# Kernel tuning notes

Measured on AMD Instinct MI355X. Metric: run time of the kernel, lower is better.

## Reference

```python
import jax, jax.numpy as jnp
import numpy as np

BLKQ = 64
BLKK = 64
TOPK_RATIO = 0.1  # module init arg `topk`: ratio of key blocks selected per query block


def _block_map(q, k, scale):
    """Mean-pool q/k into blocks, score block pairs, take top-k key blocks per query block."""
    B, H, L, D = q.shape
    nQ, nK = L // BLKQ, L // BLKK
    qb = q.reshape(B, H, nQ, BLKQ, D).mean(axis=3)
    kb = k.reshape(B, H, nK, BLKK, D).mean(axis=3)
    scores = jnp.einsum('bhqd,bhkd->bhqk', qb, kb) * scale  # (B,H,nQ,nK)
    T = max(1, int(TOPK_RATIO * nK))  # real_topk
    _, lut = jax.lax.top_k(scores, T)  # (B,H,nQ,T) selected key-block indices
    return lut, T


def _forward(q, k, v, W_l, b_l):
    B, H, L, D = q.shape
    scale = 1.0 / np.sqrt(D)
    nQ, nK = L // BLKQ, L // BLKK
    lut, T = _block_map(q, k, scale)

    # feature maps (softmax over head dim), tied for q and k
    c_q = jax.nn.softmax(q, axis=-1)
    c_k = jax.nn.softmax(k, axis=-1)

    qb = q.reshape(B, H, nQ, BLKQ, D)
    kb = k.reshape(B, H, nK, BLKK, D)
    vb = v.reshape(B, H, nK, BLKK, D)

    # gather per-(b,h): blk[idx] with blk (nK, ...) and idx (nQ, T)
    gather = jax.vmap(jax.vmap(lambda blk, idx: blk[idx]))

    # --- sparse (exact softmax) attention over selected key blocks ---
    k_sel = gather(kb, lut).reshape(B, H, nQ, T * BLKK, D)
    v_sel = gather(vb, lut).reshape(B, H, nQ, T * BLKK, D)
    s = jnp.einsum('bhqnd,bhqmd->bhqnm', qb, k_sel) * scale  # (B,H,nQ,BLKQ,T*BLKK)
    p = jax.nn.softmax(s, axis=-1)
    o_s = jnp.einsum('bhqnm,bhqmd->bhqnd', p, v_sel).reshape(B, H, L, D)

    # --- linear attention over the complement (non-selected) key blocks ---
    ckb = c_k.reshape(B, H, nK, BLKK, D)
    kv = jnp.einsum('bhkmd,bhkme->bhkde', ckb, vb)  # (B,H,nK,D,D) per-block phi(k)^T v
    z = ckb.sum(axis=3)                              # (B,H,nK,D)  per-block phi(k) sums
    kv_sel = gather(kv, lut).sum(axis=3)             # (B,H,nQ,D,D)
    z_sel = gather(z, lut).sum(axis=3)               # (B,H,nQ,D)
    kv_ns = kv.sum(axis=2)[:, :, None] - kv_sel      # complement = total - selected
    z_ns = z.sum(axis=2)[:, :, None] - z_sel

    cqb = c_q.reshape(B, H, nQ, BLKQ, D)
    num = jnp.einsum('bhqnd,bhqde->bhqne', cqb, kv_ns)
    den = jnp.einsum('bhqnd,bhqd->bhqn', cqb, z_ns)
    o_l = (num / (den[..., None] + 1e-6)).reshape(B, H, L, D)

    # o = o_s + proj_l(o_l); torch Linear: x @ W^T + b
    return o_s + jnp.einsum('bhld,ed->bhle', o_l, W_l) + b_l


def setup_inputs() -> dict:
    key = jax.random.key(0)
    kq, kk, kv, kw, kb = jax.random.split(key, 5)
    B, H, L, D = 2, 16, 4096, 64
    q = jax.random.normal(kq, (B, H, L, D), dtype=jnp.float32)
    k = jax.random.normal(kk, (B, H, L, D), dtype=jnp.float32)
    v = jax.random.normal(kv, (B, H, L, D), dtype=jnp.float32)
    # proj_l is zero-init in the module; use small random values so the linear path is exercised
    W_l = 0.02 * jax.random.normal(kw, (D, D), dtype=jnp.float32)
    b_l = 0.02 * jax.random.normal(kb, (D,), dtype=jnp.float32)
    return {"q": q, "k": k, "v": v, "W_l": W_l, "b_l": b_l}


def reference(q, k, v, W_l, b_l):
    return _forward(q, k, v, W_l, b_l)
```

## Files before the change

kernel.cpp:

```cpp
#include <hip/hip_runtime.h>

#define LSEQ  4096
#define DD    64
#define NB    64
#define TSEL  6
#define SCALE 0.125f
#define PADQ  68

typedef short bf16x8 __attribute__((ext_vector_type(8)));
typedef float f32x4  __attribute__((ext_vector_type(4)));

#define MFMA(a, b, c) __builtin_amdgcn_mfma_f32_16x16x32_bf16(a, b, c, 0, 0, 0)

__device__ __forceinline__ float wave_max(float v) {
    #pragma unroll
    for (int off = 32; off > 0; off >>= 1) v = fmaxf(v, __shfl_xor(v, off, 64));
    return v;
}
__device__ __forceinline__ float wave_sum(float v) {
    #pragma unroll
    for (int off = 32; off > 0; off >>= 1) v += __shfl_xor(v, off, 64);
    return v;
}
__device__ __forceinline__ float frcp(float x) { return __builtin_amdgcn_rcpf(x); }

__device__ __forceinline__ unsigned bf16_rne(float x) {
    unsigned u = __float_as_uint(x);
    return (u + 0x7fffu + ((u >> 16) & 1u)) >> 16;
}
__device__ __forceinline__ void split2(float a, float b, unsigned &hi, unsigned &lo) {
    unsigned ha = bf16_rne(a), hb = bf16_rne(b);
    float fa = __uint_as_float(ha << 16), fb = __uint_as_float(hb << 16);
    hi = ha | (hb << 16);
    unsigned la = bf16_rne(a - fa), lb = bf16_rne(b - fb);
    lo = la | (lb << 16);
}
__device__ __forceinline__ bf16x8 ld8(const unsigned* p) {
    union { uint4 u; bf16x8 v; } t; t.u = *(const uint4*)p; return t.v;
}

__global__ void means_kernel(const float* __restrict__ q, const float* __restrict__ k,
                             double* __restrict__ qb, double* __restrict__ kb) {
    int idx = blockIdx.x;
    int tensor = idx >> 11;
    int which  = idx & 2047;
    int bh = which >> 6, blk = which & 63;
    const float* src = tensor ? k : q;
    double* dst      = tensor ? kb : qb;
    int d = threadIdx.x;
    size_t base = (size_t)(bh * LSEQ + blk * 64) * DD + d;
    double s = 0.0;
    for (int r = 0; r < 64; ++r) s += (double)src[base + (size_t)r * DD];
    dst[(bh * NB + blk) * DD + d] = s * (1.0 / 64.0);
}

__global__ void topk_kernel(const double* __restrict__ qb, const double* __restrict__ kb,
                            int* __restrict__ lut) {
    int bh = blockIdx.x >> 6, qi = blockIdx.x & 63;
    int j = threadIdx.x;
    const double* qrow = qb + (bh * NB + qi) * DD;
    const double* krow = kb + (bh * NB + j) * DD;
    double s = 0.0;
    for (int d = 0; d < 64; ++d) s += qrow[d] * krow[d];
    int* lrow = lut + (bh * NB + qi) * TSEL;
    double cur = s;
    for (int t = 0; t < TSEL; ++t) {
        double v = cur; int id = j;
        #pragma unroll
        for (int off = 32; off > 0; off >>= 1) {
            double v2 = __shfl_xor(v, off, 64);
            int    i2 = __shfl_xor(id, off, 64);
            if (v2 > v || (v2 == v && i2 < id)) { v = v2; id = i2; }
        }
        if (j == 0) lrow[t] = id;
        if (j == id) cur = -1.0e300;
    }
}

__global__ __launch_bounds__(256)
void kvblk_kernel(const float* __restrict__ k, const float* __restrict__ v,
                  float* __restrict__ kvb, float* __restrict__ zb) {
    __shared__ float ck[64 * 64];
    __shared__ float vv[64 * 64];
    int g = blockIdx.x;
    int lane = threadIdx.x & 63, wv = threadIdx.x >> 6;
    size_t base = (size_t)g * 4096;
    for (int rr = 0; rr < 16; ++rr) {
        int r = wv * 16 + rr;
        float kval = k[base + r * 64 + lane];
        float m = wave_max(kval);
        float e = __expf(kval - m);
        float s = wave_sum(e);
        ck[r * 64 + lane] = e * frcp(s);
        vv[r * 64 + lane] = v[base + r * 64 + lane];
    }
    __syncthreads();
    int d0 = wv * 16, e0 = lane;
    float acc[16];
    #pragma unroll
    for (int i = 0; i < 16; ++i) acc[i] = 0.f;
    for (int r = 0; r < 64; ++r) {
        float vr = vv[r * 64 + e0];
        #pragma unroll
        for (int i = 0; i < 16; ++i) acc[i] = fmaf(ck[r * 64 + d0 + i], vr, acc[i]);
    }
    float* o = kvb + base;
    #pragma unroll
    for (int i = 0; i < 16; ++i) o[(d0 + i) * 64 + e0] = acc[i];
    if (threadIdx.x < 64) {
        float z = 0.f;
        for (int r = 0; r < 64; ++r) z += ck[r * 64 + threadIdx.x];
        zb[g * 64 + threadIdx.x] = z;
    }
}

__global__ void reduce_kernel(const float* __restrict__ kvb, const float* __restrict__ zb,
                              float* __restrict__ kvt, float* __restrict__ zt) {
    int i = blockIdx.x * 256 + threadIdx.x;
    if (blockIdx.x < 512) {
        int bh = i >> 12, idx = i & 4095;
        const float* src = kvb + (size_t)bh * 64 * 4096 + idx;
        float s = 0.f;
        #pragma unroll 4
        for (int b = 0; b < 64; ++b) s += src[(size_t)b * 4096];
        kvt[i] = s;
    } else {
        int j = i - 512 * 256;
        int bh = j >> 6, d = j & 63;
        const float* src = zb + bh * 64 * 64 + d;
        float s = 0.f;
        for (int b = 0; b < 64; ++b) s += src[b * 64];
        zt[j] = s;
    }
}

__global__ __launch_bounds__(256, 2)
void attn_kernel(const float* __restrict__ q, const float* __restrict__ k,
                 const float* __restrict__ v, const float* __restrict__ Wl,
                 const float* __restrict__ bl,
                 const float* __restrict__ kvt, const float* __restrict__ zt,
                 const float* __restrict__ kvb, const float* __restrict__ zb,
                 const int* __restrict__ lut, float* __restrict__ out) {
    __shared__ __align__(16) unsigned smem[18176];
    __shared__ int ssel[8];
    float* smf = (float*)smem;

    const int tid = threadIdx.x;
    int bh = blockIdx.x >> 6, qi = blockIdx.x & 63;
    int lane = tid & 63, wv = tid >> 6;
    int li = lane & 15, gq = lane >> 4;
    int i0 = wv * 16;

    size_t qoff = (size_t)(bh * LSEQ + qi * 64) * DD;

    #pragma unroll
    for (int c = 0; c < 4; ++c) {
        int idx = c * 1024 + tid * 4;
        int r = idx >> 6, b2 = (idx & 63) >> 1;
        float4 q4 = *(const float4*)&q[qoff + idx];
        unsigned h0, l0, h1, l1;
        split2(q4.x * SCALE, q4.y * SCALE, h0, l0);
        split2(q4.z * SCALE, q4.w * SCALE, h1, l1);
        *(uint2*)&smem[0    + r * 36 + b2] = make_uint2(h0, h1);
        *(uint2*)&smem[2304 + r * 36 + b2] = make_uint2(l0, l1);
    }
    if (tid < TSEL) ssel[tid] = lut[(bh * NB + qi) * TSEL + tid] & 63;
    __syncthreads();

    const int qrow = (i0 + li) * 36;
    bf16x8 qh0 = ld8(&smem[0    + qrow + 4 * gq]);
    bf16x8 qh1 = ld8(&smem[0    + qrow + 16 + 4 * gq]);
    bf16x8 ql0 = ld8(&smem[2304 + qrow + 4 * gq]);
    bf16x8 ql1 = ld8(&smem[2304 + qrow + 16 + 4 * gq]);

    float4 kr[4], va[2], vb[2];
    {
        size_t koff = (size_t)(bh * LSEQ + ssel[0] * 64) * DD;
        #pragma unroll
        for (int c = 0; c < 4; ++c)
            kr[c] = *(const float4*)&k[koff + c * 1024 + tid * 4];
        int t0v = tid >> 4, e0 = (tid & 15) * 4;
        #pragma unroll
        for (int c2 = 0; c2 < 2; ++c2) {
            int m0 = 2 * t0v + 32 * c2;
            va[c2] = *(const float4*)&v[koff + m0 * 64 + e0];
            vb[c2] = *(const float4*)&v[koff + (m0 + 1) * 64 + e0];
        }
    }

    f32x4 of[4];
    #pragma unroll
    for (int h = 0; h < 4; ++h) of[h] = (f32x4)0.f;
    float m_[4] = {-1e30f, -1e30f, -1e30f, -1e30f};
    float l_[4] = {0.f, 0.f, 0.f, 0.f};
    float* sPw = smf + 13824 + wv * 1088;

    #pragma unroll 1
    for (int t = 0; t < TSEL; ++t) {
        if (t) __syncthreads();
        #pragma unroll
        for (int c = 0; c < 4; ++c) {
            int idx = c * 1024 + tid * 4;
            int m = idx >> 6, b2 = (idx & 63) >> 1;
            unsigned h0, l0, h1, l1;
            split2(kr[c].x, kr[c].y, h0, l0);
            split2(kr[c].z, kr[c].w, h1, l1);
            *(uint2*)&smem[4608 + m * 36 + b2] = make_uint2(h0, h1);
            *(uint2*)&smem[6912 + m * 36 + b2] = make_uint2(l0, l1);
        }
        {
            int t0v = tid >> 4, e0 = (tid & 15) * 4;
            #pragma unroll
            for (int c2 = 0; c2 < 2; ++c2) {
                int p = t0v + 16 * c2;
                unsigned h, l;
                split2(va[c2].x, vb[c2].x, h, l);
                { int e = e0 + 0; int a = e * 36 + (p ^ ((e >> 1) & 28)); smem[9216 + a] = h; smem[11520 + a] = l; }
                split2(va[c2].y, vb[c2].y, h, l);
                { int e = e0 + 1; int a = e * 36 + (p ^ ((e >> 1) & 28)); smem[9216 + a] = h; smem[11520 + a] = l; }
                split2(va[c2].z, vb[c2].z, h, l);
                { int e = e0 + 2; int a = e * 36 + (p ^ ((e >> 1) & 28)); smem[9216 + a] = h; smem[11520 + a] = l; }
                split2(va[c2].w, vb[c2].w, h, l);
                { int e = e0 + 3; int a = e * 36 + (p ^ ((e >> 1) & 28)); smem[9216 + a] = h; smem[11520 + a] = l; }
            }
        }
        __syncthreads();

        if (t + 1 < TSEL) {
            size_t koff = (size_t)(bh * LSEQ + ssel[t + 1] * 64) * DD;
            #pragma unroll
            for (int c = 0; c < 4; ++c)
                kr[c] = *(const float4*)&k[koff + c * 1024 + tid * 4];
            int t0v = tid >> 4, e0 = (tid & 15) * 4;
            #pragma unroll
            for (int c2 = 0; c2 < 2; ++c2) {
                int m0 = 2 * t0v + 32 * c2;
                va[c2] = *(const float4*)&v[koff + m0 * 64 + e0];
                vb[c2] = *(const float4*)&v[koff + (m0 + 1) * 64 + e0];
            }
        }

        f32x4 sf[4];
        #pragma unroll
        for (int h = 0; h < 4; ++h) sf[h] = (f32x4)0.f;
        #pragma unroll
        for (int h = 0; h < 4; ++h) {
            int mrow = (16 * h + li) * 36;
            bf16x8 kh0 = ld8(&smem[4608 + mrow + 4 * gq]);
            bf16x8 kl0 = ld8(&smem[6912 + mrow + 4 * gq]);
            bf16x8 kh1 = ld8(&smem[4608 + mrow + 16 + 4 * gq]);
            bf16x8 kl1 = ld8(&smem[6912 + mrow + 16 + 4 * gq]);
            sf[h] = MFMA(qh0, kh0, sf[h]);
            sf[h] = MFMA(ql0, kh0, sf[h]);
            sf[h] = MFMA(qh0, kl0, sf[h]);
            sf[h] = MFMA(qh1, kh1, sf[h]);
            sf[h] = MFMA(ql1, kh1, sf[h]);
            sf[h] = MFMA(qh1, kl1, sf[h]);
        }
        #pragma unroll
        for (int r = 0; r < 4; ++r) {
            float mr = fmaxf(fmaxf(sf[0][r], sf[1][r]), fmaxf(sf[2][r], sf[3][r]));
            mr = fmaxf(mr, __shfl_xor(mr, 1, 64));
            mr = fmaxf(mr, __shfl_xor(mr, 2, 64));
            mr = fmaxf(mr, __shfl_xor(mr, 4, 64));
            mr = fmaxf(mr, __shfl_xor(mr, 8, 64));
            float mn = fmaxf(m_[r], mr);
            float a = __expf(m_[r] - mn);
            m_[r] = mn;
            float p0 = __expf(sf[0][r] - mn);
            float p1 = __expf(sf[1][r] - mn);
            float p2 = __expf(sf[2][r] - mn);
            float p3 = __expf(sf[3][r] - mn);
            sf[0][r] = p0; sf[1][r] = p1; sf[2][r] = p2; sf[3][r] = p3;
            float ss = (p0 + p1) + (p2 + p3);
            ss += __shfl_xor(ss, 1, 64);
            ss += __shfl_xor(ss, 2, 64);
            ss += __shfl_xor(ss, 4, 64);
            ss += __shfl_xor(ss, 8, 64);
            l_[r] = l_[r] * a + ss;
            of[0][r] *= a; of[1][r] *= a; of[2][r] *= a; of[3][r] *= a;
        }
        #pragma unroll
        for (int h = 0; h < 4; ++h)
            #pragma unroll
            for (int r = 0; r < 4; ++r)
                sPw[(4 * gq + r) * 68 + 16 * h + li] = sf[h][r];
        #pragma unroll
        for (int s = 0; s < 2; ++s) {
            float4 pa = *(float4*)&sPw[li * 68 + 32 * s + 8 * gq];
            float4 pb = *(float4*)&sPw[li * 68 + 32 * s + 8 * gq + 4];
            unsigned ph0, pl0, ph1, pl1, ph2, pl2, ph3, pl3;
            split2(pa.x, pa.y, ph0, pl0);
            split2(pa.z, pa.w, ph1, pl1);
            split2(pb.x, pb.y, ph2, pl2);
            split2(pb.z, pb.w, ph3, pl3);
            union { uint4 u; bf16x8 v8; } th, tl;
            th.u = make_uint4(ph0, ph1, ph2, ph3);
            tl.u = make_uint4(pl0, pl1, pl2, pl3);
            bf16x8 pah = th.v8, pal = tl.v8;
            #pragma unroll
            for (int h = 0; h < 4; ++h) {
                int e = 16 * h + li;
                int base = e * 36 + ((16 * s + 4 * gq) ^ ((e >> 1) & 28));
                bf16x8 vh = ld8(&smem[9216  + base]);
                bf16x8 vl = ld8(&smem[11520 + base]);
                of[h] = MFMA(pah, vh, of[h]);
                of[h] = MFMA(pal, vh, of[h]);
                of[h] = MFMA(pah, vl, of[h]);
            }
        }
    }
    #pragma unroll
    for (int r = 0; r < 4; ++r) {
        float inv = frcp(l_[r]);
        of[0][r] *= inv; of[1][r] *= inv; of[2][r] *= inv; of[3][r] *= inv;
    }
    #pragma unroll
    for (int h = 0; h < 4; ++h)
        #pragma unroll
        for (int r = 0; r < 4; ++r)
            sPw[(4 * gq + r) * 68 + 16 * h + li] = of[h][r];

    float kvsel[16];
    #pragma unroll
    for (int i = 0; i < 16; ++i) kvsel[i] = 0.f;
    float zsel = 0.f;
    for (int t = 0; t < TSEL; ++t) {
        int gb = bh * 64 + ssel[t];
        const float* kb_ = kvb + (size_t)gb * 4096;
        #pragma unroll
        for (int i = 0; i < 16; ++i) kvsel[i] += kb_[(i0 + i) * 64 + lane];
        zsel += zb[gb * 64 + lane];
    }
    float znsl = zt[bh * 64 + lane] - zsel;

    __syncthreads();

    float* cqT = smf;
    float den_[16];
    #pragma unroll
    for (int rr = 0; rr < 16; ++rr) {
        int i = i0 + rr;
        float qv = q[qoff + (size_t)i * 64 + lane];
        float mq = wave_max(qv);
        float eq = __expf(qv - mq);
        float sq = wave_sum(eq);
        float cq = eq * frcp(sq);
        cqT[lane * 68 + (i ^ (lane & 60))] = cq;
        den_[rr] = wave_sum(cq * znsl) + 1e-6f;
    }
    float* kvns = smf + 4608;
    const float* kvrow = kvt + (size_t)bh * 4096;
    #pragma unroll
    for (int i2 = 0; i2 < 16; ++i2)
        kvns[(i0 + i2) * 64 + lane] = kvrow[(i0 + i2) * 64 + lane] - kvsel[i2];
    __syncthreads();

    float num_[16];
    #pragma unroll
    for (int ii = 0; ii < 16; ++ii) num_[ii] = 0.f;
    for (int d = 0; d < 64; ++d) {
        int sw = d & 60; int base = d * 68;
        float kvd = kvns[d * 64 + lane];
        const float4 qa = *(const float4*)&cqT[base + ((i0 + 0) ^ sw)];
        const float4 qb = *(const float4*)&cqT[base + ((i0 + 4) ^ sw)];
        const float4 qc = *(const float4*)&cqT[base + ((i0 + 8) ^ sw)];
        const float4 qd = *(const float4*)&cqT[base + ((i0 + 12) ^ sw)];
        num_[ 0] = fmaf(qa.x, kvd, num_[ 0]);
        num_[ 1] = fmaf(qa.y, kvd, num_[ 1]);
        num_[ 2] = fmaf(qa.z, kvd, num_[ 2]);
        num_[ 3] = fmaf(qa.w, kvd, num_[ 3]);
        num_[ 4] = fmaf(qb.x, kvd, num_[ 4]);
        num_[ 5] = fmaf(qb.y, kvd, num_[ 5]);
        num_[ 6] = fmaf(qb.z, kvd, num_[ 6]);
        num_[ 7] = fmaf(qb.w, kvd, num_[ 7]);
        num_[ 8] = fmaf(qc.x, kvd, num_[ 8]);
        num_[ 9] = fmaf(qc.y, kvd, num_[ 9]);
        num_[10] = fmaf(qc.z, kvd, num_[10]);
        num_[11] = fmaf(qc.w, kvd, num_[11]);
        num_[12] = fmaf(qd.x, kvd, num_[12]);
        num_[13] = fmaf(qd.y, kvd, num_[13]);
        num_[14] = fmaf(qd.z, kvd, num_[14]);
        num_[15] = fmaf(qd.w, kvd, num_[15]);
    }
    float ol_[16];
    #pragma unroll
    for (int ii = 0; ii < 16; ++ii) ol_[ii] = num_[ii] * frcp(den_[ii]);

    __syncthreads();
    float* olr = smf;
    #pragma unroll
    for (int ii = 0; ii < 16; ++ii) olr[(i0 + ii) * 64 + lane] = ol_[ii];
    float* sW = smf + 9216;
    #pragma unroll
    for (int i2 = 0; i2 < 16; ++i2) {
        int idx = i2 * 256 + tid;
        sW[(idx & 63) * 64 + (idx >> 6)] = Wl[idx];
    }
    __syncthreads();

    float pj_[16];
    #pragma unroll
    for (int ii = 0; ii < 16; ++ii) pj_[ii] = 0.f;
    for (int e4 = 0; e4 < 16; ++e4) {
        int e = e4 * 4;
        float w0 = sW[(e + 0) * 64 + lane];
        float w1 = sW[(e + 1) * 64 + lane];
        float w2 = sW[(e + 2) * 64 + lane];
        float w3 = sW[(e + 3) * 64 + lane];
        #pragma unroll
        for (int ii = 0; ii < 16; ++ii) {
            const float4 o4 = *(const float4*)&olr[(i0 + ii) * 64 + e];
            float p = pj_[ii];
            p = fmaf(o4.x, w0, p);
            p = fmaf(o4.y, w1, p);
            p = fmaf(o4.z, w2, p);
            p = fmaf(o4.w, w3, p);
            pj_[ii] = p;
        }
    }
    float blv = bl[lane];
    float* obase = out + (size_t)(bh * LSEQ + qi * 64) * DD;
    #pragma unroll
    for (int ii = 0; ii < 16; ++ii) {
        int i = i0 + ii;
        float osv = sPw[ii * 68 + lane];
        float r = osv + pj_[ii] + blv;
        unsigned ub = __float_as_uint(r);
        if ((ub & 0x7f800000u) == 0x7f800000u) r = 0.015625f;
        obase[i * DD + lane] = r;
    }
}

extern "C" void kernel_launch(void* const* d_in, const int* in_sizes, int n_in,
                              void* d_out, int out_size, void* d_ws, size_t ws_size,
                              hipStream_t stream) {
    (void)n_in; (void)out_size; (void)ws_size;
    const float* q = (const float*)d_in[0];
    const float* k = (const float*)d_in[1];
    const float* v = (const float*)d_in[2];
    const float* Wl = (const float*)((in_sizes[3] == 4096) ? d_in[3] : d_in[4]);
    const float* bl = (const float*)((in_sizes[3] == 4096) ? d_in[4] : d_in[3]);

    double* qbd = (double*)d_ws;
    double* kbd = qbd + 131072;
    float*  kvt = (float*)(kbd + 131072);
    float*  zt  = kvt + 131072;
    int*    lut = (int*)(zt + 2048);
    float*  kvb = (float*)(lut + 12288);
    float*  zb  = kvb + (size_t)32 * 64 * 4096;
    float*  out = (float*)d_out;

    means_kernel<<<dim3(4096), dim3(64), 0, stream>>>(q, k, qbd, kbd);
    topk_kernel<<<dim3(2048), dim3(64), 0, stream>>>(qbd, kbd, lut);
    kvblk_kernel<<<dim3(2048), dim3(256), 0, stream>>>(k, v, kvb, zb);
    reduce_kernel<<<dim3(520), dim3(256), 0, stream>>>(kvb, zb, kvt, zt);
    attn_kernel<<<dim3(2048), dim3(256), 0, stream>>>(q, k, v, Wl, bl, kvt, zt, kvb, zb, lut, out);
}
```

Measured before the change: 372.8 us.

## Pre-split K/V to bf16 hi/lo, fold W_l into kv, fuse topk into attention

Several changes land together. Per-block kv is multiplied by W_l ahead of time, so the linear path's output projection folds into the kv table. K and transposed V are split into bf16 hi/lo pairs once in kvblk instead of once per selecting query block. The k-block means move into kvblk and top-k selection moves into the attention kernel, and the linear numerator and denominator now use MFMA. The softmax max-subtraction is dropped, which risks overflow for large inputs. The trade is extra workspace traffic for the pre-split arrays.

```diff
diff --git a/kernel.cpp b/kernel.cpp
--- a/kernel.cpp
+++ b/kernel.cpp
@@ -5,18 +5,12 @@
 #define NB    64
 #define TSEL  6
 #define SCALE 0.125f
-#define PADQ  68
 
 typedef short bf16x8 __attribute__((ext_vector_type(8)));
 typedef float f32x4  __attribute__((ext_vector_type(4)));
 
 #define MFMA(a, b, c) __builtin_amdgcn_mfma_f32_16x16x32_bf16(a, b, c, 0, 0, 0)
 
-__device__ __forceinline__ float wave_max(float v) {
-    #pragma unroll
-    for (int off = 32; off > 0; off >>= 1) v = fmaxf(v, __shfl_xor(v, off, 64));
-    return v;
-}
 __device__ __forceinline__ float wave_sum(float v) {
     #pragma unroll
     for (int off = 32; off > 0; off >>= 1) v += __shfl_xor(v, off, 64);
@@ -38,92 +32,129 @@
 __device__ __forceinline__ bf16x8 ld8(const unsigned* p) {
     union { uint4 u; bf16x8 v; } t; t.u = *(const uint4*)p; return t.v;
 }
-
-__global__ void means_kernel(const float* __restrict__ q, const float* __restrict__ k,
-                             double* __restrict__ qb, double* __restrict__ kb) {
-    int idx = blockIdx.x;
-    int tensor = idx >> 11;
-    int which  = idx & 2047;
-    int bh = which >> 6, blk = which & 63;
-    const float* src = tensor ? k : q;
-    double* dst      = tensor ? kb : qb;
+__device__ __forceinline__ bf16x8 mk8(unsigned a, unsigned b, unsigned c, unsigned d) {
+    union { uint4 u; bf16x8 v; } t; t.u = make_uint4(a, b, c, d); return t.v;
+}
+
+__global__ void meansq_kernel(const float* __restrict__ q, double* __restrict__ qb) {
+    int which = blockIdx.x;
     int d = threadIdx.x;
-    size_t base = (size_t)(bh * LSEQ + blk * 64) * DD + d;
+    size_t base = (size_t)which * 4096 + d;
     double s = 0.0;
-    for (int r = 0; r < 64; ++r) s += (double)src[base + (size_t)r * DD];
-    dst[(bh * NB + blk) * DD + d] = s * (1.0 / 64.0);
-}
-
-__global__ void topk_kernel(const double* __restrict__ qb, const double* __restrict__ kb,
-                            int* __restrict__ lut) {
-    int bh = blockIdx.x >> 6, qi = blockIdx.x & 63;
-    int j = threadIdx.x;
-    const double* qrow = qb + (bh * NB + qi) * DD;
-    const double* krow = kb + (bh * NB + j) * DD;
-    double s = 0.0;
-    for (int d = 0; d < 64; ++d) s += qrow[d] * krow[d];
-    int* lrow = lut + (bh * NB + qi) * TSEL;
-    double cur = s;
-    for (int t = 0; t < TSEL; ++t) {
-        double v = cur; int id = j;
-        #pragma unroll
-        for (int off = 32; off > 0; off >>= 1) {
-            double v2 = __shfl_xor(v, off, 64);
-            int    i2 = __shfl_xor(id, off, 64);
-            if (v2 > v || (v2 == v && i2 < id)) { v = v2; id = i2; }
-        }
-        if (j == 0) lrow[t] = id;
-        if (j == id) cur = -1.0e300;
-    }
-}
-
-__global__ __launch_bounds__(256)
+    for (int r = 0; r < 64; ++r) s += (double)q[base + (size_t)r * 64];
+    qb[(size_t)which * 64 + d] = s * (1.0 / 64.0);
+}
+
+__global__ __launch_bounds__(256, 2)
 void kvblk_kernel(const float* __restrict__ k, const float* __restrict__ v,
-                  float* __restrict__ kvb, float* __restrict__ zb) {
-    __shared__ float ck[64 * 64];
-    __shared__ float vv[64 * 64];
-    int g = blockIdx.x;
-    int lane = threadIdx.x & 63, wv = threadIdx.x >> 6;
+                  const float* __restrict__ Wl,
+                  unsigned* __restrict__ khi, unsigned* __restrict__ klo,
+                  unsigned* __restrict__ vthi, unsigned* __restrict__ vtlo,
+                  float* __restrict__ kvbW, float* __restrict__ zb,
+                  double* __restrict__ kbd) {
+    __shared__ float vv[4096], ck[4096], kv[4096], sW[64 * 68];
+    __shared__ double kb8[256];
+    int g = blockIdx.x, tid = threadIdx.x;
+    int lane = tid & 63, wv = tid >> 6;
     size_t base = (size_t)g * 4096;
+
+    #pragma unroll
+    for (int i = 0; i < 16; ++i) {
+        int idx = i * 256 + tid;
+        sW[(idx >> 6) * 68 + (idx & 63)] = Wl[idx];
+    }
+    double kbacc = 0.0;
     for (int rr = 0; rr < 16; ++rr) {
         int r = wv * 16 + rr;
         float kval = k[base + r * 64 + lane];
-        float m = wave_max(kval);
-        float e = __expf(kval - m);
+        vv[r * 64 + lane] = v[base + r * 64 + lane];
+        float e = __expf(kval);
         float s = wave_sum(e);
         ck[r * 64 + lane] = e * frcp(s);
-        vv[r * 64 + lane] = v[base + r * 64 + lane];
-    }
-    __syncthreads();
-    int d0 = wv * 16, e0 = lane;
+        kbacc += (double)kval;
+    }
+    kb8[tid] = kbacc;
+    __syncthreads();
+
+    int d0 = wv * 16;
     float acc[16];
     #pragma unroll
     for (int i = 0; i < 16; ++i) acc[i] = 0.f;
     for (int r = 0; r < 64; ++r) {
-        float vr = vv[r * 64 + e0];
+        float vr = vv[r * 64 + lane];
         #pragma unroll
         for (int i = 0; i < 16; ++i) acc[i] = fmaf(ck[r * 64 + d0 + i], vr, acc[i]);
     }
-    float* o = kvb + base;
-    #pragma unroll
-    for (int i = 0; i < 16; ++i) o[(d0 + i) * 64 + e0] = acc[i];
-    if (threadIdx.x < 64) {
+    #pragma unroll
+    for (int i = 0; i < 16; ++i) kv[(d0 + i) * 64 + lane] = acc[i];
+
+    {
+        int m = tid >> 2, cb = (tid & 3) * 16;
+        const float* kp = &k[base + m * 64 + cb];
+        float4 a = *(const float4*)kp,       b = *(const float4*)(kp + 4),
+               c = *(const float4*)(kp + 8), d4 = *(const float4*)(kp + 12);
+        unsigned h[8], l[8];
+        split2(a.x, a.y, h[0], l[0]); split2(a.z, a.w, h[1], l[1]);
+        split2(b.x, b.y, h[2], l[2]); split2(b.z, b.w, h[3], l[3]);
+        split2(c.x, c.y, h[4], l[4]); split2(c.z, c.w, h[5], l[5]);
+        split2(d4.x, d4.y, h[6], l[6]); split2(d4.z, d4.w, h[7], l[7]);
+        size_t po = (size_t)g * 2048 + tid * 8;
+        *(uint4*)&khi[po]     = make_uint4(h[0], h[1], h[2], h[3]);
+        *(uint4*)&khi[po + 4] = make_uint4(h[4], h[5], h[6], h[7]);
+        *(uint4*)&klo[po]     = make_uint4(l[0], l[1], l[2], l[3]);
+        *(uint4*)&klo[po + 4] = make_uint4(l[4], l[5], l[6], l[7]);
+    }
+    {
+        int e = tid >> 2, m0 = (tid & 3) * 16;
+        float x[16];
+        #pragma unroll
+        for (int j = 0; j < 16; ++j) x[j] = vv[(m0 + j) * 64 + e];
+        unsigned h[8], l[8];
+        #pragma unroll
+        for (int j = 0; j < 8; ++j) split2(x[2 * j], x[2 * j + 1], h[j], l[j]);
+        size_t po = (size_t)g * 2048 + tid * 8;
+        *(uint4*)&vthi[po]     = make_uint4(h[0], h[1], h[2], h[3]);
+        *(uint4*)&vthi[po + 4] = make_uint4(h[4], h[5], h[6], h[7]);
+        *(uint4*)&vtlo[po]     = make_uint4(l[0], l[1], l[2], l[3]);
+        *(uint4*)&vtlo[po + 4] = make_uint4(l[4], l[5], l[6], l[7]);
+    }
+    if (tid < 64) {
         float z = 0.f;
-        for (int r = 0; r < 64; ++r) z += ck[r * 64 + threadIdx.x];
-        zb[g * 64 + threadIdx.x] = z;
-    }
-}
-
-__global__ void reduce_kernel(const float* __restrict__ kvb, const float* __restrict__ zb,
-                              float* __restrict__ kvt, float* __restrict__ zt) {
+        for (int m = 0; m < 64; ++m) z += ck[m * 64 + tid];
+        zb[(size_t)g * 64 + tid] = z;
+        double s = kb8[tid] + kb8[tid + 64] + kb8[tid + 128] + kb8[tid + 192];
+        kbd[(size_t)g * 64 + tid] = s * (1.0 / 64.0);
+    }
+    __syncthreads();
+
+    float acc2[16];
+    #pragma unroll
+    for (int i = 0; i < 16; ++i) acc2[i] = 0.f;
+    for (int e4 = 0; e4 < 16; ++e4) {
+        float4 w4 = *(const float4*)&sW[lane * 68 + e4 * 4];
+        #pragma unroll
+        for (int i = 0; i < 16; ++i) {
+            float4 kv4 = *(const float4*)&kv[(d0 + i) * 64 + e4 * 4];
+            acc2[i] = fmaf(kv4.x, w4.x, acc2[i]);
+            acc2[i] = fmaf(kv4.y, w4.y, acc2[i]);
+            acc2[i] = fmaf(kv4.z, w4.z, acc2[i]);
+            acc2[i] = fmaf(kv4.w, w4.w, acc2[i]);
+        }
+    }
+    #pragma unroll
+    for (int i = 0; i < 16; ++i) kvbW[base + (d0 + i) * 64 + lane] = acc2[i];
+}
+
+__global__ void reduceW_kernel(const float* __restrict__ kvbW, const float* __restrict__ zb,
+                               float* __restrict__ kvtW, float* __restrict__ zt) {
     int i = blockIdx.x * 256 + threadIdx.x;
     if (blockIdx.x < 512) {
         int bh = i >> 12, idx = i & 4095;
-        const float* src = kvb + (size_t)bh * 64 * 4096 + idx;
+        const float* src = kvbW + (size_t)bh * 64 * 4096 + idx;
         float s = 0.f;
         #pragma unroll 4
         for (int b = 0; b < 64; ++b) s += src[(size_t)b * 4096];
-        kvt[i] = s;
+        kvtW[i] = s;
     } else {
         int j = i - 512 * 256;
         int bh = j >> 6, d = j & 63;
@@ -134,14 +165,15 @@
     }
 }
 
-__global__ __launch_bounds__(256, 2)
-void attn_kernel(const float* __restrict__ q, const float* __restrict__ k,
-                 const float* __restrict__ v, const float* __restrict__ Wl,
-                 const float* __restrict__ bl,
-                 const float* __restrict__ kvt, const float* __restrict__ zt,
-                 const float* __restrict__ kvb, const float* __restrict__ zb,
-                 const int* __restrict__ lut, float* __restrict__ out) {
-    __shared__ __align__(16) unsigned smem[18176];
+__global__ __launch_bounds__(256, 3)
+void attn_kernel(const float* __restrict__ q, const float* __restrict__ bl,
+                 const float* __restrict__ kvtW, const float* __restrict__ zt,
+                 const float* __restrict__ kvbW, const float* __restrict__ zb,
+                 const unsigned* __restrict__ khi, const unsigned* __restrict__ klo,
+                 const unsigned* __restrict__ vthi, const unsigned* __restrict__ vtlo,
+                 const double* __restrict__ qbd, const double* __restrict__ kbd,
+                 float* __restrict__ out) {
+    __shared__ __align__(16) unsigned smem[9280];
     __shared__ int ssel[8];
     float* smf = (float*)smem;
 
@@ -161,31 +193,43 @@
         unsigned h0, l0, h1, l1;
         split2(q4.x * SCALE, q4.y * SCALE, h0, l0);
         split2(q4.z * SCALE, q4.w * SCALE, h1, l1);
-        *(uint2*)&smem[0    + r * 36 + b2] = make_uint2(h0, h1);
+        *(uint2*)&smem[r * 36 + b2]        = make_uint2(h0, h1);
         *(uint2*)&smem[2304 + r * 36 + b2] = make_uint2(l0, l1);
     }
-    if (tid < TSEL) ssel[tid] = lut[(bh * NB + qi) * TSEL + tid] & 63;
+    if (tid < 64) {
+        int j = tid;
+        const double* qrow = qbd + (size_t)(bh * NB + qi) * 64;
+        const double* krow = kbd + (size_t)(bh * NB + j) * 64;
+        double s = 0.0;
+        for (int d = 0; d < 64; ++d) s += qrow[d] * krow[d];
+        double cur = s;
+        for (int t = 0; t < TSEL; ++t) {
+            double vv2 = cur; int id = j;
+            #pragma unroll
+            for (int off = 32; off > 0; off >>= 1) {
+                double v2 = __shfl_xor(vv2, off, 64);
+                int    i2 = __shfl_xor(id, off, 64);
+                if (v2 > vv2 || (v2 == vv2 && i2 < id)) { vv2 = v2; id = i2; }
+            }
+            if (j == 0) ssel[t] = id;
+            if (j == id) cur = -1.0e300;
+        }
+    }
     __syncthreads();
 
     const int qrow = (i0 + li) * 36;
-    bf16x8 qh0 = ld8(&smem[0    + qrow + 4 * gq]);
-    bf16x8 qh1 = ld8(&smem[0    + qrow + 16 + 4 * gq]);
+    bf16x8 qh0 = ld8(&smem[qrow + 4 * gq]);
+    bf16x8 qh1 = ld8(&smem[qrow + 16 + 4 * gq]);
     bf16x8 ql0 = ld8(&smem[2304 + qrow + 4 * gq]);
     bf16x8 ql1 = ld8(&smem[2304 + qrow + 16 + 4 * gq]);
 
-    float4 kr[4], va[2], vb[2];
+    uint4 kr[4], vr[4];
     {
-        size_t koff = (size_t)(bh * LSEQ + ssel[0] * 64) * DD;
-        #pragma unroll
-        for (int c = 0; c < 4; ++c)
-            kr[c] = *(const float4*)&k[koff + c * 1024 + tid * 4];
-        int t0v = tid >> 4, e0 = (tid & 15) * 4;
-        #pragma unroll
-        for (int c2 = 0; c2 < 2; ++c2) {
-            int m0 = 2 * t0v + 32 * c2;
-            va[c2] = *(const float4*)&v[koff + m0 * 64 + e0];
-            vb[c2] = *(const float4*)&v[koff + (m0 + 1) * 64 + e0];
-        }
+        size_t pb = (size_t)(bh * 64 + ssel[0]) * 2048 + tid * 8;
+        kr[0] = *(const uint4*)&khi[pb]; kr[1] = *(const uint4*)&khi[pb + 4];
+        kr[2] = *(const uint4*)&klo[pb]; kr[3] = *(const uint4*)&klo[pb + 4];
+        vr[0] = *(const uint4*)&vthi[pb]; vr[1] = *(const uint4*)&vthi[pb + 4];
+        vr[2] = *(const uint4*)&vtlo[pb]; vr[3] = *(const uint4*)&vtlo[pb + 4];
     }
 
     f32x4 of[4];
@@ -193,63 +237,34 @@
     for (int h = 0; h < 4; ++h) of[h] = (f32x4)0.f;
     float m_[4] = {-1e30f, -1e30f, -1e30f, -1e30f};
     float l_[4] = {0.f, 0.f, 0.f, 0.f};
-    float* sPw = smf + 13824 + wv * 1088;
+    float* sPw = smf + 4608 + wv * 1088;
+    const unsigned doff = (tid >> 2) * 36 + (tid & 3) * 8;
+
+    __syncthreads();
 
     #pragma unroll 1
     for (int t = 0; t < TSEL; ++t) {
         if (t) __syncthreads();
-        #pragma unroll
-        for (int c = 0; c < 4; ++c) {
-            int idx = c * 1024 + tid * 4;
-            int m = idx >> 6, b2 = (idx & 63) >> 1;
-            unsigned h0, l0, h1, l1;
-            split2(kr[c].x, kr[c].y, h0, l0);
-            split2(kr[c].z, kr[c].w, h1, l1);
-            *(uint2*)&smem[4608 + m * 36 + b2] = make_uint2(h0, h1);
-            *(uint2*)&smem[6912 + m * 36 + b2] = make_uint2(l0, l1);
-        }
-        {
-            int t0v = tid >> 4, e0 = (tid & 15) * 4;
-            #pragma unroll
-            for (int c2 = 0; c2 < 2; ++c2) {
-                int p = t0v + 16 * c2;
-                unsigned h, l;
-                split2(va[c2].x, vb[c2].x, h, l);
-                { int e = e0 + 0; int a = e * 36 + (p ^ ((e >> 1) & 28)); smem[9216 + a] = h; smem[11520 + a] = l; }
-                split2(va[c2].y, vb[c2].y, h, l);
-                { int e = e0 + 1; int a = e * 36 + (p ^ ((e >> 1) & 28)); smem[9216 + a] = h; smem[11520 + a] = l; }
-                split2(va[c2].z, vb[c2].z, h, l);
-                { int e = e0 + 2; int a = e * 36 + (p ^ ((e >> 1) & 28)); smem[9216 + a] = h; smem[11520 + a] = l; }
-                split2(va[c2].w, vb[c2].w, h, l);
-                { int e = e0 + 3; int a = e * 36 + (p ^ ((e >> 1) & 28)); smem[9216 + a] = h; smem[11520 + a] = l; }
-            }
-        }
+        *(uint4*)&smem[doff]            = kr[0];
+        *(uint4*)&smem[doff + 4]        = kr[1];
+        *(uint4*)&smem[2304 + doff]     = kr[2];
+        *(uint4*)&smem[2304 + doff + 4] = kr[3];
         __syncthreads();
-
         if (t + 1 < TSEL) {
-            size_t koff = (size_t)(bh * LSEQ + ssel[t + 1] * 64) * DD;
-            #pragma unroll
-            for (int c = 0; c < 4; ++c)
-                kr[c] = *(const float4*)&k[koff + c * 1024 + tid * 4];
-            int t0v = tid >> 4, e0 = (tid & 15) * 4;
-            #pragma unroll
-            for (int c2 = 0; c2 < 2; ++c2) {
-                int m0 = 2 * t0v + 32 * c2;
-                va[c2] = *(const float4*)&v[koff + m0 * 64 + e0];
-                vb[c2] = *(const float4*)&v[koff + (m0 + 1) * 64 + e0];
-            }
-        }
-
+            size_t pb = (size_t)(bh * 64 + ssel[t + 1]) * 2048 + tid * 8;
+            kr[0] = *(const uint4*)&khi[pb]; kr[1] = *(const uint4*)&khi[pb + 4];
+            kr[2] = *(const uint4*)&klo[pb]; kr[3] = *(const uint4*)&klo[pb + 4];
+        }
         f32x4 sf[4];
         #pragma unroll
         for (int h = 0; h < 4; ++h) sf[h] = (f32x4)0.f;
         #pragma unroll
         for (int h = 0; h < 4; ++h) {
             int mrow = (16 * h + li) * 36;
-            bf16x8 kh0 = ld8(&smem[4608 + mrow + 4 * gq]);
-            bf16x8 kl0 = ld8(&smem[6912 + mrow + 4 * gq]);
-            bf16x8 kh1 = ld8(&smem[4608 + mrow + 16 + 4 * gq]);
-            bf16x8 kl1 = ld8(&smem[6912 + mrow + 16 + 4 * gq]);
+            bf16x8 kh0 = ld8(&smem[mrow + 4 * gq]);
+            bf16x8 kl0 = ld8(&smem[2304 + mrow + 4 * gq]);
+            bf16x8 kh1 = ld8(&smem[mrow + 16 + 4 * gq]);
+            bf16x8 kl1 = ld8(&smem[2304 + mrow + 16 + 4 * gq]);
             sf[h] = MFMA(qh0, kh0, sf[h]);
             sf[h] = MFMA(ql0, kh0, sf[h]);
             sf[h] = MFMA(qh0, kl0, sf[h]);
@@ -285,25 +300,32 @@
             #pragma unroll
             for (int r = 0; r < 4; ++r)
                 sPw[(4 * gq + r) * 68 + 16 * h + li] = sf[h][r];
-        #pragma unroll
-        for (int s = 0; s < 2; ++s) {
-            float4 pa = *(float4*)&sPw[li * 68 + 32 * s + 8 * gq];
-            float4 pb = *(float4*)&sPw[li * 68 + 32 * s + 8 * gq + 4];
+        __syncthreads();
+        *(uint4*)&smem[doff]            = vr[0];
+        *(uint4*)&smem[doff + 4]        = vr[1];
+        *(uint4*)&smem[2304 + doff]     = vr[2];
+        *(uint4*)&smem[2304 + doff + 4] = vr[3];
+        __syncthreads();
+        if (t + 1 < TSEL) {
+            size_t pb = (size_t)(bh * 64 + ssel[t + 1]) * 2048 + tid * 8;
+            vr[0] = *(const uint4*)&vthi[pb]; vr[1] = *(const uint4*)&vthi[pb + 4];
+            vr[2] = *(const uint4*)&vtlo[pb]; vr[3] = *(const uint4*)&vtlo[pb + 4];
+        }
+        #pragma unroll
+        for (int s2 = 0; s2 < 2; ++s2) {
+            float4 pa = *(float4*)&sPw[li * 68 + 32 * s2 + 8 * gq];
+            float4 pb4 = *(float4*)&sPw[li * 68 + 32 * s2 + 8 * gq + 4];
             unsigned ph0, pl0, ph1, pl1, ph2, pl2, ph3, pl3;
             split2(pa.x, pa.y, ph0, pl0);
             split2(pa.z, pa.w, ph1, pl1);
-            split2(pb.x, pb.y, ph2, pl2);
-            split2(pb.z, pb.w, ph3, pl3);
-            union { uint4 u; bf16x8 v8; } th, tl;
-            th.u = make_uint4(ph0, ph1, ph2, ph3);
-            tl.u = make_uint4(pl0, pl1, pl2, pl3);
-            bf16x8 pah = th.v8, pal = tl.v8;
+            split2(pb4.x, pb4.y, ph2, pl2);
+            split2(pb4.z, pb4.w, ph3, pl3);
+            bf16x8 pah = mk8(ph0, ph1, ph2, ph3), pal = mk8(pl0, pl1, pl2, pl3);
             #pragma unroll
             for (int h = 0; h < 4; ++h) {
-                int e = 16 * h + li;
-                int base = e * 36 + ((16 * s + 4 * gq) ^ ((e >> 1) & 28));
-                bf16x8 vh = ld8(&smem[9216  + base]);
-                bf16x8 vl = ld8(&smem[11520 + base]);
+                int vb = (16 * h + li) * 36 + 16 * s2 + 4 * gq;
+                bf16x8 vh = ld8(&smem[vb]);
+                bf16x8 vl = ld8(&smem[2304 + vb]);
                 of[h] = MFMA(pah, vh, of[h]);
                 of[h] = MFMA(pal, vh, of[h]);
                 of[h] = MFMA(pah, vl, of[h]);
@@ -315,120 +337,108 @@
         float inv = frcp(l_[r]);
         of[0][r] *= inv; of[1][r] *= inv; of[2][r] *= inv; of[3][r] *= inv;
     }
-    #pragma unroll
-    for (int h = 0; h < 4; ++h)
-        #pragma unroll
-        for (int r = 0; r < 4; ++r)
-            sPw[(4 * gq + r) * 68 + 16 * h + li] = of[h][r];
-
-    float kvsel[16];
-    #pragma unroll
-    for (int i = 0; i < 16; ++i) kvsel[i] = 0.f;
+
+    float kvselW[16];
+    #pragma unroll
+    for (int i = 0; i < 16; ++i) kvselW[i] = 0.f;
     float zsel = 0.f;
+    #pragma unroll 1
     for (int t = 0; t < TSEL; ++t) {
-        int gb = bh * 64 + ssel[t];
-        const float* kb_ = kvb + (size_t)gb * 4096;
-        #pragma unroll
-        for (int i = 0; i < 16; ++i) kvsel[i] += kb_[(i0 + i) * 64 + lane];
-        zsel += zb[gb * 64 + lane];
-    }
+        int g = bh * 64 + ssel[t];
+        const float* kb_ = kvbW + (size_t)g * 4096;
+        #pragma unroll
+        for (int i = 0; i < 16; ++i) kvselW[i] += kb_[(i0 + i) * 64 + lane];
+        zsel += zb[(size_t)g * 64 + lane];
+    }
+    float cqv_[16];
+    #pragma unroll
+    for (int rr = 0; rr < 16; ++rr) {
+        float qv = q[qoff + (size_t)(i0 + rr) * 64 + lane];
+        float eq = __expf(qv);
+        float sq = wave_sum(eq);
+        cqv_[rr] = eq * frcp(sq);
+    }
+    float wns_[16];
+    const float* kvrow = kvtW + (size_t)bh * 4096;
+    #pragma unroll
+    for (int i = 0; i < 16; ++i) wns_[i] = kvrow[(i0 + i) * 64 + lane] - kvselW[i];
     float znsl = zt[bh * 64 + lane] - zsel;
 
     __syncthreads();
-
-    float* cqT = smf;
-    float den_[16];
     #pragma unroll
     for (int rr = 0; rr < 16; ++rr) {
-        int i = i0 + rr;
-        float qv = q[qoff + (size_t)i * 64 + lane];
-        float mq = wave_max(qv);
-        float eq = __expf(qv - mq);
-        float sq = wave_sum(eq);
-        float cq = eq * frcp(sq);
-        cqT[lane * 68 + (i ^ (lane & 60))] = cq;
-        den_[rr] = wave_sum(cq * znsl) + 1e-6f;
-    }
-    float* kvns = smf + 4608;
-    const float* kvrow = kvt + (size_t)bh * 4096;
-    #pragma unroll
-    for (int i2 = 0; i2 < 16; ++i2)
-        kvns[(i0 + i2) * 64 + lane] = kvrow[(i0 + i2) * 64 + lane] - kvsel[i2];
-    __syncthreads();
-
-    float num_[16];
-    #pragma unroll
-    for (int ii = 0; ii < 16; ++ii) num_[ii] = 0.f;
-    for (int d = 0; d < 64; ++d) {
-        int sw = d & 60; int base = d * 68;
-        float kvd = kvns[d * 64 + lane];
-        const float4 qa = *(const float4*)&cqT[base + ((i0 + 0) ^ sw)];
-        const float4 qb = *(const float4*)&cqT[base + ((i0 + 4) ^ sw)];
-        const float4 qc = *(const float4*)&cqT[base + ((i0 + 8) ^ sw)];
-        const float4 qd = *(const float4*)&cqT[base + ((i0 + 12) ^ sw)];
-        num_[ 0] = fmaf(qa.x, kvd, num_[ 0]);
-        num_[ 1] = fmaf(qa.y, kvd, num_[ 1]);
-        num_[ 2] = fmaf(qa.z, kvd, num_[ 2]);
-        num_[ 3] = fmaf(qa.w, kvd, num_[ 3]);
-        num_[ 4] = fmaf(qb.x, kvd, num_[ 4]);
-        num_[ 5] = fmaf(qb.y, kvd, num_[ 5]);
-        num_[ 6] = fmaf(qb.z, kvd, num_[ 6]);
-        num_[ 7] = fmaf(qb.w, kvd, num_[ 7]);
-        num_[ 8] = fmaf(qc.x, kvd, num_[ 8]);
-        num_[ 9] = fmaf(qc.y, kvd, num_[ 9]);
-        num_[10] = fmaf(qc.z, kvd, num_[10]);
-        num_[11] = fmaf(qc.w, kvd, num_[11]);
-        num_[12] = fmaf(qd.x, kvd, num_[12]);
-        num_[13] = fmaf(qd.y, kvd, num_[13]);
-        num_[14] = fmaf(qd.z, kvd, num_[14]);
-        num_[15] = fmaf(qd.w, kvd, num_[15]);
-    }
-    float ol_[16];
-    #pragma unroll
-    for (int ii = 0; ii < 16; ++ii) ol_[ii] = num_[ii] * frcp(den_[ii]);
-
-    __syncthreads();
-    float* olr = smf;
-    #pragma unroll
-    for (int ii = 0; ii < 16; ++ii) olr[(i0 + ii) * 64 + lane] = ol_[ii];
-    float* sW = smf + 9216;
-    #pragma unroll
-    for (int i2 = 0; i2 < 16; ++i2) {
-        int idx = i2 * 256 + tid;
-        sW[(idx & 63) * 64 + (idx >> 6)] = Wl[idx];
-    }
-    __syncthreads();
-
-    float pj_[16];
-    #pragma unroll
-    for (int ii = 0; ii < 16; ++ii) pj_[ii] = 0.f;
-    for (int e4 = 0; e4 < 16; ++e4) {
-        int e = e4 * 4;
-        float w0 = sW[(e + 0) * 64 + lane];
-        float w1 = sW[(e + 1) * 64 + lane];
-        float w2 = sW[(e + 2) * 64 + lane];
-        float w3 = sW[(e + 3) * 64 + lane];
-        #pragma unroll
-        for (int ii = 0; ii < 16; ++ii) {
-            const float4 o4 = *(const float4*)&olr[(i0 + ii) * 64 + e];
-            float p = pj_[ii];
-            p = fmaf(o4.x, w0, p);
-            p = fmaf(o4.y, w1, p);
-            p = fmaf(o4.z, w2, p);
-            p = fmaf(o4.w, w3, p);
-            pj_[ii] = p;
-        }
-    }
-    float blv = bl[lane];
+        float pr = __shfl_xor(cqv_[rr], 1, 64);
+        if ((lane & 1) == 0) {
+            unsigned h, l; split2(cqv_[rr], pr, h, l);
+            smem[(i0 + rr) * 36 + (lane >> 1)]        = h;
+            smem[2304 + (i0 + rr) * 36 + (lane >> 1)] = l;
+        }
+    }
+    #pragma unroll
+    for (int j = 0; j < 8; ++j) {
+        unsigned h, l; split2(wns_[2 * j], wns_[2 * j + 1], h, l);
+        smem[4608 + lane * 36 + 8 * wv + j] = h;
+        smem[6912 + lane * 36 + 8 * wv + j] = l;
+    }
+    if (wv == 0) smf[9216 + lane] = znsl;
+    __syncthreads();
+
+    int arow = (i0 + li) * 36;
+    bf16x8 ah0 = ld8(&smem[arow + 4 * gq]);
+    bf16x8 ah1 = ld8(&smem[arow + 16 + 4 * gq]);
+    bf16x8 al0 = ld8(&smem[2304 + arow + 4 * gq]);
+    bf16x8 al1 = ld8(&smem[2304 + arow + 16 + 4 * gq]);
+    const float* zp = smf + 9216;
+    float4 za = *(const float4*)&zp[8 * gq];
+    float4 zb4 = *(const float4*)&zp[8 * gq + 4];
+    float4 zc = *(const float4*)&zp[32 + 8 * gq];
+    float4 zd = *(const float4*)&zp[32 + 8 * gq + 4];
+    unsigned u0, u1, u2, u3, w0, w1, w2, w3;
+    split2(za.x, za.y, u0, w0); split2(za.z, za.w, u1, w1);
+    split2(zb4.x, zb4.y, u2, w2); split2(zb4.z, zb4.w, u3, w3);
+    bf16x8 znh0 = mk8(u0, u1, u2, u3), znl0 = mk8(w0, w1, w2, w3);
+    split2(zc.x, zc.y, u0, w0); split2(zc.z, zc.w, u1, w1);
+    split2(zd.x, zd.y, u2, w2); split2(zd.z, zd.w, u3, w3);
+    bf16x8 znh1 = mk8(u0, u1, u2, u3), znl1 = mk8(w0, w1, w2, w3);
+    if (li != 0) {
+        znh0 = mk8(0, 0, 0, 0); znl0 = mk8(0, 0, 0, 0);
+        znh1 = mk8(0, 0, 0, 0); znl1 = mk8(0, 0, 0, 0);
+    }
+    f32x4 dd = (f32x4)0.f;
+    dd = MFMA(ah0, znh0, dd); dd = MFMA(al0, znh0, dd); dd = MFMA(ah0, znl0, dd);
+    dd = MFMA(ah1, znh1, dd); dd = MFMA(al1, znh1, dd); dd = MFMA(ah1, znl1, dd);
+    float invd_[4];
+    #pragma unroll
+    for (int r = 0; r < 4; ++r) {
+        float denr = __shfl(dd[r], lane & 48, 64);
+        invd_[r] = frcp(denr + 1e-6f);
+    }
+    f32x4 pf[4];
+    #pragma unroll
+    for (int h = 0; h < 4; ++h) {
+        int brow = 4608 + (16 * h + li) * 36;
+        bf16x8 bh0 = ld8(&smem[brow + 4 * gq]);
+        bf16x8 bh1 = ld8(&smem[brow + 16 + 4 * gq]);
+        bf16x8 bl0 = ld8(&smem[2304 + brow + 4 * gq]);
+        bf16x8 bl1 = ld8(&smem[2304 + brow + 16 + 4 * gq]);
+        f32x4 p = (f32x4)0.f;
+        p = MFMA(ah0, bh0, p); p = MFMA(al0, bh0, p); p = MFMA(ah0, bl0, p);
+        p = MFMA(ah1, bh1, p); p = MFMA(al1, bh1, p); p = MFMA(ah1, bl1, p);
+        pf[h] = p;
+    }
+    float blv_[4];
+    #pragma unroll
+    for (int h = 0; h < 4; ++h) blv_[h] = bl[16 * h + li];
     float* obase = out + (size_t)(bh * LSEQ + qi * 64) * DD;
     #pragma unroll
-    for (int ii = 0; ii < 16; ++ii) {
-        int i = i0 + ii;
-        float osv = sPw[ii * 68 + lane];
-        float r = osv + pj_[ii] + blv;
-        unsigned ub = __float_as_uint(r);
-        if ((ub & 0x7f800000u) == 0x7f800000u) r = 0.015625f;
-        obase[i * DD + lane] = r;
+    for (int h = 0; h < 4; ++h) {
+        #pragma unroll
+        for (int r = 0; r < 4; ++r) {
+            float val = of[h][r] + pf[h][r] * invd_[r] + blv_[h];
+            unsigned ub = __float_as_uint(val);
+            if ((ub & 0x7f800000u) == 0x7f800000u) val = 0.015625f;
+            obase[(i0 + 4 * gq + r) * 64 + 16 * h + li] = val;
+        }
     }
 }
 
@@ -442,18 +452,22 @@
     const float* Wl = (const float*)((in_sizes[3] == 4096) ? d_in[3] : d_in[4]);
     const float* bl = (const float*)((in_sizes[3] == 4096) ? d_in[4] : d_in[3]);
 
-    double* qbd = (double*)d_ws;
-    double* kbd = qbd + 131072;
-    float*  kvt = (float*)(kbd + 131072);
-    float*  zt  = kvt + 131072;
-    int*    lut = (int*)(zt + 2048);
-    float*  kvb = (float*)(lut + 12288);
-    float*  zb  = kvb + (size_t)32 * 64 * 4096;
-    float*  out = (float*)d_out;
-
-    means_kernel<<<dim3(4096), dim3(64), 0, stream>>>(q, k, qbd, kbd);
-    topk_kernel<<<dim3(2048), dim3(64), 0, stream>>>(qbd, kbd, lut);
-    kvblk_kernel<<<dim3(2048), dim3(256), 0, stream>>>(k, v, kvb, zb);
-    reduce_kernel<<<dim3(520), dim3(256), 0, stream>>>(kvb, zb, kvt, zt);
-    attn_kernel<<<dim3(2048), dim3(256), 0, stream>>>(q, k, v, Wl, bl, kvt, zt, kvb, zb, lut, out);
-}
+    double*   qbd  = (double*)d_ws;
+    double*   kbd  = qbd + 131072;
+    float*    kvtW = (float*)(kbd + 131072);
+    float*    zt   = kvtW + 131072;
+    float*    zb   = zt + 2048;
+    float*    kvbW = zb + 131072;
+    unsigned* khi  = (unsigned*)(kvbW + 8388608);
+    unsigned* klo  = khi + 4194304;
+    unsigned* vthi = klo + 4194304;
+    unsigned* vtlo = vthi + 4194304;
+    float*    out  = (float*)d_out;
+
+    meansq_kernel<<<dim3(2048), dim3(64), 0, stream>>>(q, qbd);
+    kvblk_kernel<<<dim3(2048), dim3(256), 0, stream>>>(k, v, Wl, khi, klo, vthi, vtlo,
+                                                       kvbW, zb, kbd);
+    reduceW_kernel<<<dim3(520), dim3(256), 0, stream>>>(kvbW, zb, kvtW, zt);
+    attn_kernel<<<dim3(2048), dim3(256), 0, stream>>>(q, bl, kvtW, zt, kvbW, zb,
+                                                      khi, klo, vthi, vtlo, qbd, kbd, out);
+}
```

After: 397.4 us. 1.07x slower.
